# Optimization experiments

Hardware: AMD Instinct MI355X
Metric: run time of the kernel (lower is better)

Reference implementation:

```python
import jax, jax.numpy as jnp
import numpy as np

N, E, F, B, S, T, D = 50000, 150000, 100000, 64, 32, 32, 3
RADIUS = 1.0
SCALE = 500.0


def setup_inputs() -> dict:
    key = jax.random.key(0)
    ks = jax.random.split(key, 8)
    x = jax.random.normal(ks[0], (N, D), dtype=jnp.float32)
    node_weights = jax.random.uniform(ks[1], (N,), dtype=jnp.float32)
    edge_index = jax.random.randint(ks[2], (2, E), 0, N)
    edge_weights = jax.random.uniform(ks[3], (E,), dtype=jnp.float32)
    face = jax.random.randint(ks[4], (3, F), 0, N)
    face_weights = jax.random.uniform(ks[5], (F,), dtype=jnp.float32)
    batch = jnp.sort(jax.random.randint(ks[6], (N,), 0, B))
    v = jax.random.normal(ks[7], (D, T), dtype=jnp.float32)
    v = v / jnp.linalg.norm(v, axis=0, keepdims=True)  # unit directions
    lin = jnp.linspace(-RADIUS, RADIUS, S, dtype=jnp.float32)
    return {"x": x, "node_weights": node_weights, "edge_index": edge_index,
            "edge_weights": edge_weights, "face": face, "face_weights": face_weights,
            "batch": batch, "v": v, "lin": lin}


def compute_ecc(h, index, lin, num_segments):
    # h: [M, T] simplex heights; lin: [S] thresholds
    # sigmoid bump at each threshold, then scatter-add per graph -> [B, S, T]
    ecc = jax.nn.sigmoid(SCALE * (lin[None, :, None] - h[:, None, :]))  # [M, S, T]
    return jax.ops.segment_sum(ecc, index, num_segments=num_segments)


def reference(x, node_weights, edge_index, edge_weights, face, face_weights, batch, v, lin):
    nh = (x * node_weights[:, None]) @ v                      # [N, T] node heights
    eh = jnp.max(nh[edge_index], axis=0) * edge_weights[:, None]  # [E, T]
    fh = jnp.max(nh[face], axis=0) * face_weights[:, None]        # [F, T]
    idx_e = batch[edge_index[0]]
    idx_f = batch[face[0]]
    ect = (compute_ecc(nh, batch, lin, B)
           - compute_ecc(eh, idx_e, lin, B)
           + compute_ecc(fh, idx_f, lin, B))                  # [B, S, T]
    return ect  # normalized=False -> squeeze() is a no-op here
```

## Files before the change

kernel.cpp:

```cpp
#include <hip/hip_runtime.h>
#include <hip/hip_bf16.h>

#define N_NODES 50000
#define N_EDGES 150000
#define N_FACES 100000
#define NB 64
#define NS 32
#define NT 32
#define SCALE_C 500.0f
#define DLIN (2.0f / 31.0f)
#define INV_DLIN (31.0f / 2.0f)
#define WIN 0.02f
#define DSZ (NB * NS * NT)
#define NODE_CAP 1024
#define EDGE_CAP 3072
#define FACE_CAP 2048
#define SENT_H 2.0f

__device__ __forceinline__ float sigf(float z) {
    float e = __expf(-z);
    return __builtin_amdgcn_rcpf(1.0f + e);
}
__device__ __forceinline__ float4 fmax4(float4 a, float4 b) {
    return make_float4(fmaxf(a.x,b.x), fmaxf(a.y,b.y), fmaxf(a.z,b.z), fmaxf(a.w,b.w));
}
__device__ __forceinline__ float4 fscale4(float4 a, float w) {
    return make_float4(a.x*w, a.y*w, a.z*w, a.w*w);
}

__global__ __launch_bounds__(256) void fill_kernel(
    float* __restrict__ nh, int* __restrict__ ns,
    int* __restrict__ ea, int* __restrict__ eb, float* __restrict__ ews,
    int* __restrict__ fa, int* __restrict__ fb, int* __restrict__ fc,
    float* __restrict__ fws)
{
    int i = blockIdx.x * 256 + threadIdx.x;
    if (i < NT) nh[N_NODES * NT + i] = SENT_H;
    if (i < NB * NODE_CAP) ns[i] = N_NODES;
    if (i < NB * EDGE_CAP) { ea[i] = N_NODES; eb[i] = N_NODES; ews[i] = 1.0f; }
    if (i < NB * FACE_CAP) { fa[i] = N_NODES; fb[i] = N_NODES; fc[i] = N_NODES; fws[i] = 1.0f; }
}

__global__ __launch_bounds__(256) void prep_kernel(
    const float* __restrict__ x, const float* __restrict__ nw,
    const float* __restrict__ v, const int* __restrict__ ei,
    const float* __restrict__ ew, const int* __restrict__ fi,
    const float* __restrict__ fw, const int* __restrict__ batch,
    float* __restrict__ nh, int* __restrict__ ns,
    int* __restrict__ ea, int* __restrict__ eb, float* __restrict__ ews,
    int* __restrict__ fa, int* __restrict__ fb, int* __restrict__ fc,
    float* __restrict__ fws, int* __restrict__ cur,
    int nhB, int nbN, int nbE)
{
    if (blockIdx.x < nhB) {
        int idx = blockIdx.x * 256 + threadIdx.x;
        if (idx < N_NODES * NT) {
            int n = idx >> 5, t = idx & 31;
            float w = nw[n];
            nh[idx] = w * (x[3 * n] * v[t] + x[3 * n + 1] * v[NT + t] + x[3 * n + 2] * v[2 * NT + t]);
        }
        return;
    }
    __shared__ int cnt[NB], base_[NB];
    int b = blockIdx.x - nhB;
    int type, bb, M;
    if (b < nbN)            { type = 0; bb = b;             M = N_NODES; }
    else if (b < nbN + nbE) { type = 1; bb = b - nbN;       M = N_EDGES; }
    else                    { type = 2; bb = b - nbN - nbE; M = N_FACES; }
    int c0 = bb * 1024;
    if (threadIdx.x < NB) cnt[threadIdx.x] = 0;
    __syncthreads();
    int gv[4], iv[4], n = 0;
    #pragma unroll
    for (int k = 0; k < 4; k++) {
        int i = c0 + k * 256 + threadIdx.x;
        if (i < M) {
            int first = (type == 0) ? i : (type == 1 ? ei[i] : fi[i]);
            gv[n] = batch[first];
            iv[n] = i;
            atomicAdd(&cnt[gv[n]], 1);
            n++;
        }
    }
    __syncthreads();
    int* curT = cur + type * NB;
    if (threadIdx.x < NB) {
        base_[threadIdx.x] = atomicAdd(&curT[threadIdx.x], cnt[threadIdx.x]);
        cnt[threadIdx.x] = 0;
    }
    __syncthreads();
    int CAP = (type == 0) ? NODE_CAP : (type == 1 ? EDGE_CAP : FACE_CAP);
    for (int k = 0; k < n; k++) {
        int g = gv[k], i = iv[k];
        int pos = g * CAP + base_[g] + atomicAdd(&cnt[g], 1);
        if (type == 0) {
            ns[pos] = i;
        } else if (type == 1) {
            ea[pos] = ei[i]; eb[pos] = ei[N_EDGES + i]; ews[pos] = ew[i];
        } else {
            fa[pos] = fi[i]; fb[pos] = fi[N_FACES + i];
            fc[pos] = fi[2 * N_FACES + i]; fws[pos] = fw[i];
        }
    }
}

__global__ __launch_bounds__(256) void accum_kernel(
    const float* __restrict__ nh, const int* __restrict__ ns,
    const int* __restrict__ ea, const int* __restrict__ eb,
    const float* __restrict__ ews, const int* __restrict__ fa,
    const int* __restrict__ fb, const int* __restrict__ fc,
    const float* __restrict__ fws, const int* __restrict__ cur,
    float* __restrict__ delta)
{
    const int NBN = NB * NODE_CAP / 256;
    const int NBE = NB * EDGE_CAP / 256;
    int bid = blockIdx.x;
    int type, g, base, end;
    float sign;
    if (bid < NBN) {
        type = 0; g = bid >> 2; base = g * NODE_CAP + (bid & 3) * 256;
        end = g * NODE_CAP + cur[g]; sign = 1.0f;
    } else if (bid < NBN + NBE) {
        int b = bid - NBN; type = 1; g = b / 12;
        base = g * EDGE_CAP + (b % 12) * 256;
        end = g * EDGE_CAP + cur[NB + g]; sign = -1.0f;
    } else {
        int b = bid - NBN - NBE; type = 2; g = b >> 3;
        base = g * FACE_CAP + (b & 7) * 256;
        end = g * FACE_CAP + cur[2 * NB + g]; sign = 1.0f;
    }
    if (base >= end) return;

    __shared__ float tile[NT * NS];
    for (int k = threadIdx.x; k < NT * NS; k += 256) tile[k] = 0.0f;
    __syncthreads();

    int sub = threadIdx.x & 3;
    int sid = threadIdx.x >> 2;
    int t0 = sub * 8;

    #pragma unroll
    for (int p = 0; p < 4; p++) {
        int i = base + p * 64 + sid;
        float4 r0, r1;
        if (type == 0) {
            const float4* row = (const float4*)(nh + ns[i] * NT + t0);
            r0 = row[0]; r1 = row[1];
        } else if (type == 1) {
            const float4* ra = (const float4*)(nh + ea[i] * NT + t0);
            const float4* rb = (const float4*)(nh + eb[i] * NT + t0);
            float w = ews[i];
            float4 a0 = ra[0], a1 = ra[1], b0 = rb[0], b1 = rb[1];
            r0 = fscale4(fmax4(a0, b0), w);
            r1 = fscale4(fmax4(a1, b1), w);
        } else {
            const float4* ra = (const float4*)(nh + fa[i] * NT + t0);
            const float4* rb = (const float4*)(nh + fb[i] * NT + t0);
            const float4* rc = (const float4*)(nh + fc[i] * NT + t0);
            float w = fws[i];
            float4 a0 = ra[0], a1 = ra[1], b0 = rb[0], b1 = rb[1], c0 = rc[0], c1 = rc[1];
            r0 = fscale4(fmax4(fmax4(a0, b0), c0), w);
            r1 = fscale4(fmax4(fmax4(a1, b1), c1), w);
        }
        float h[8] = {r0.x, r0.y, r0.z, r0.w, r1.x, r1.y, r1.z, r1.w};
        #pragma unroll
        for (int j = 0; j < 8; j++) {
            float hh = h[j];
            int slo_u = (int)ceilf((hh - WIN + 1.0f) * INV_DLIN);
            int shi_u = (int)floorf((hh + WIN + 1.0f) * INV_DLIN);
            int slo = slo_u < 0 ? 0 : slo_u;
            int shi = shi_u > (NS - 1) ? (NS - 1) : shi_u;
            float prev = 0.0f;
            for (int s = slo; s <= shi; s++) {
                float vs = sigf(SCALE_C * (-1.0f + s * DLIN - hh));
                atomicAdd(&tile[(t0 + j) * NS + s], vs - prev);
                prev = vs;
            }
            int sstep = shi_u + 1;
            if (sstep <= NS - 1) {
                int sc = sstep < 0 ? 0 : sstep;
                atomicAdd(&tile[(t0 + j) * NS + sc], 1.0f - prev);
            }
        }
    }

    __syncthreads();
    for (int k = threadIdx.x; k < NT * NS; k += 256) {
        float vv = tile[k];
        if (vv != 0.0f) {
            int tt = k >> 5, ss = k & 31;
            atomicAdd(&delta[g * (NS * NT) + ss * NT + tt], sign * vv);
        }
    }
}

__global__ void finalize_kernel(const float* __restrict__ delta, float* __restrict__ out) {
    int idx = blockIdx.x * blockDim.x + threadIdx.x;
    if (idx >= NB * NT) return;
    int g = idx >> 5, t = idx & 31;
    const float* dg = delta + (g * NS) * NT + t;
    float* og = out + (g * NS) * NT + t;
    float run = 0.0f;
    for (int s = 0; s < NS; s++) {
        run += dg[s * NT];
        og[s * NT] = run;
    }
}

extern "C" void kernel_launch(void* const* d_in, const int* in_sizes, int n_in,
                              void* d_out, int out_size, void* d_ws, size_t ws_size,
                              hipStream_t stream) {
    const float* x     = (const float*)d_in[0];
    const float* nw    = (const float*)d_in[1];
    const int*   ei    = (const int*)d_in[2];
    const float* ew    = (const float*)d_in[3];
    const int*   fi    = (const int*)d_in[4];
    const float* fw    = (const float*)d_in[5];
    const int*   batch = (const int*)d_in[6];
    const float* v     = (const float*)d_in[7];
    const float* lin   = (const float*)d_in[8];
    (void)lin; (void)in_sizes; (void)n_in; (void)ws_size;
    float* out = (float*)d_out;

    char* ws = (char*)d_ws;
    float* delta = (float*)ws;
    int*   cur   = (int*)(ws + DSZ * 4);
    float* nh    = (float*)(ws + DSZ * 4 + 1024);
    int*   ns    = (int*)((char*)nh + (size_t)(N_NODES + 1) * NT * 4);
    int*   ea    = ns + NB * NODE_CAP;
    int*   eb    = ea + NB * EDGE_CAP;
    float* ews   = (float*)(eb + NB * EDGE_CAP);
    int*   fa    = (int*)(ews + NB * EDGE_CAP);
    int*   fb    = fa + NB * FACE_CAP;
    int*   fc    = fb + NB * FACE_CAP;
    float* fws   = (float*)(fc + NB * FACE_CAP);

    hipMemsetAsync(delta, 0, DSZ * 4 + 1024, stream);

    fill_kernel<<<NB * EDGE_CAP / 256, 256, 0, stream>>>(nh, ns, ea, eb, ews, fa, fb, fc, fws);

    int nhB = (N_NODES * NT + 255) / 256;
    int nbN = (N_NODES + 1023) / 1024;
    int nbE = (N_EDGES + 1023) / 1024;
    int nbF = (N_FACES + 1023) / 1024;
    prep_kernel<<<nhB + nbN + nbE + nbF, 256, 0, stream>>>(
        x, nw, v, ei, ew, fi, fw, batch,
        nh, ns, ea, eb, ews, fa, fb, fc, fws, cur, nhB, nbN, nbE);

    int nblk = NB * (NODE_CAP + EDGE_CAP + FACE_CAP) / 256;
    accum_kernel<<<nblk, 256, 0, stream>>>(
        nh, ns, ea, eb, ews, fa, fb, fc, fws, cur, delta);

    finalize_kernel<<<(NB * NT + 255) / 256, 256, 0, stream>>>(delta, out);
}
```

Baseline: 195.1 us.

## Remap accum threads to one wave per simplex with prefetched gathers

Changes the accum kernel mapping so each wave of 32 lanes handles one simplex, one lane per direction t, instead of 4 lanes covering 8 directions each. Loads become coalesced 128-byte rows, and the next simplex's indices and heights are software-prefetched across a 32-iteration loop. The shared tile is switched to s-major so LDS atomics from a wave hit consecutive addresses, and the final flush no longer transposes. Tail padding is added to the index arrays so prefetch reads past the segment stay in bounds. The cost is more loop iterations per thread and more divergence in the per-height window loop across lanes.

```diff
diff --git a/kernel.cpp b/kernel.cpp
--- a/kernel.cpp
+++ b/kernel.cpp
@@ -15,17 +15,12 @@
 #define NODE_CAP 1024
 #define EDGE_CAP 3072
 #define FACE_CAP 2048
+#define TAILPAD 64
 #define SENT_H 2.0f
 
 __device__ __forceinline__ float sigf(float z) {
     float e = __expf(-z);
     return __builtin_amdgcn_rcpf(1.0f + e);
-}
-__device__ __forceinline__ float4 fmax4(float4 a, float4 b) {
-    return make_float4(fmaxf(a.x,b.x), fmaxf(a.y,b.y), fmaxf(a.z,b.z), fmaxf(a.w,b.w));
-}
-__device__ __forceinline__ float4 fscale4(float4 a, float w) {
-    return make_float4(a.x*w, a.y*w, a.z*w, a.w*w);
 }
 
 __global__ __launch_bounds__(256) void fill_kernel(
@@ -36,9 +31,9 @@
 {
     int i = blockIdx.x * 256 + threadIdx.x;
     if (i < NT) nh[N_NODES * NT + i] = SENT_H;
-    if (i < NB * NODE_CAP) ns[i] = N_NODES;
-    if (i < NB * EDGE_CAP) { ea[i] = N_NODES; eb[i] = N_NODES; ews[i] = 1.0f; }
-    if (i < NB * FACE_CAP) { fa[i] = N_NODES; fb[i] = N_NODES; fc[i] = N_NODES; fws[i] = 1.0f; }
+    if (i < NB * NODE_CAP + TAILPAD) ns[i] = N_NODES;
+    if (i < NB * EDGE_CAP + TAILPAD) { ea[i] = N_NODES; eb[i] = N_NODES; ews[i] = 1.0f; }
+    if (i < NB * FACE_CAP + TAILPAD) { fa[i] = N_NODES; fb[i] = N_NODES; fc[i] = N_NODES; fws[i] = 1.0f; }
 }
 
 __global__ __launch_bounds__(256) void prep_kernel(
@@ -131,66 +126,80 @@
     }
     if (base >= end) return;
 
-    __shared__ float tile[NT * NS];
-    for (int k = threadIdx.x; k < NT * NS; k += 256) tile[k] = 0.0f;
-    __syncthreads();
-
-    int sub = threadIdx.x & 3;
-    int sid = threadIdx.x >> 2;
-    int t0 = sub * 8;
-
-    #pragma unroll
-    for (int p = 0; p < 4; p++) {
-        int i = base + p * 64 + sid;
-        float4 r0, r1;
-        if (type == 0) {
-            const float4* row = (const float4*)(nh + ns[i] * NT + t0);
-            r0 = row[0]; r1 = row[1];
-        } else if (type == 1) {
-            const float4* ra = (const float4*)(nh + ea[i] * NT + t0);
-            const float4* rb = (const float4*)(nh + eb[i] * NT + t0);
-            float w = ews[i];
-            float4 a0 = ra[0], a1 = ra[1], b0 = rb[0], b1 = rb[1];
-            r0 = fscale4(fmax4(a0, b0), w);
-            r1 = fscale4(fmax4(a1, b1), w);
-        } else {
-            const float4* ra = (const float4*)(nh + fa[i] * NT + t0);
-            const float4* rb = (const float4*)(nh + fb[i] * NT + t0);
-            const float4* rc = (const float4*)(nh + fc[i] * NT + t0);
-            float w = fws[i];
-            float4 a0 = ra[0], a1 = ra[1], b0 = rb[0], b1 = rb[1], c0 = rc[0], c1 = rc[1];
-            r0 = fscale4(fmax4(fmax4(a0, b0), c0), w);
-            r1 = fscale4(fmax4(fmax4(a1, b1), c1), w);
-        }
-        float h[8] = {r0.x, r0.y, r0.z, r0.w, r1.x, r1.y, r1.z, r1.w};
-        #pragma unroll
-        for (int j = 0; j < 8; j++) {
-            float hh = h[j];
-            int slo_u = (int)ceilf((hh - WIN + 1.0f) * INV_DLIN);
-            int shi_u = (int)floorf((hh + WIN + 1.0f) * INV_DLIN);
-            int slo = slo_u < 0 ? 0 : slo_u;
-            int shi = shi_u > (NS - 1) ? (NS - 1) : shi_u;
-            float prev = 0.0f;
-            for (int s = slo; s <= shi; s++) {
-                float vs = sigf(SCALE_C * (-1.0f + s * DLIN - hh));
-                atomicAdd(&tile[(t0 + j) * NS + s], vs - prev);
-                prev = vs;
-            }
-            int sstep = shi_u + 1;
-            if (sstep <= NS - 1) {
-                int sc = sstep < 0 ? 0 : sstep;
-                atomicAdd(&tile[(t0 + j) * NS + sc], 1.0f - prev);
-            }
-        }
-    }
-
-    __syncthreads();
-    for (int k = threadIdx.x; k < NT * NS; k += 256) {
+    __shared__ float tile[NS * NT];
+    for (int k = threadIdx.x; k < NS * NT; k += 256) tile[k] = 0.0f;
+    __syncthreads();
+
+    int t = threadIdx.x & 31, slot = threadIdx.x >> 5;
+
+    #define EMIT(H) do {                                                    \
+        float hh = (H);                                                     \
+        int slo_u = (int)ceilf((hh - WIN + 1.0f) * INV_DLIN);               \
+        int shi_u = (int)floorf((hh + WIN + 1.0f) * INV_DLIN);              \
+        int slo = slo_u < 0 ? 0 : slo_u;                                    \
+        int shi = shi_u > (NS - 1) ? (NS - 1) : shi_u;                      \
+        float prev = 0.0f;                                                  \
+        for (int s = slo; s <= shi; s++) {                                  \
+            float vs = sigf(SCALE_C * (-1.0f + s * DLIN - hh));             \
+            atomicAdd(&tile[s * NT + t], vs - prev);                        \
+            prev = vs;                                                      \
+        }                                                                   \
+        int sstep = shi_u + 1;                                              \
+        if (sstep <= NS - 1) {                                              \
+            int sc = sstep < 0 ? 0 : sstep;                                 \
+            atomicAdd(&tile[sc * NT + t], 1.0f - prev);                     \
+        } } while (0)
+
+    if (type == 0) {
+        int i = base + slot;
+        int n1 = ns[i + 8];
+        float h0 = nh[ns[i] * NT + t];
+        #pragma unroll 2
+        for (int k = 0; k < 32; k++) {
+            int n2 = ns[i + 16];
+            float h1 = nh[n1 * NT + t];
+            EMIT(h0);
+            n1 = n2; h0 = h1; i += 8;
+        }
+    } else if (type == 1) {
+        int i = base + slot;
+        int a1 = ea[i + 8], b1 = eb[i + 8];
+        float w1 = ews[i + 8];
+        int a0 = ea[i], b0 = eb[i];
+        float w0 = ews[i];
+        float ha0 = nh[a0 * NT + t], hb0 = nh[b0 * NT + t];
+        #pragma unroll 2
+        for (int k = 0; k < 32; k++) {
+            int a2 = ea[i + 16], b2 = eb[i + 16];
+            float w2 = ews[i + 16];
+            float ha1 = nh[a1 * NT + t], hb1 = nh[b1 * NT + t];
+            EMIT(fmaxf(ha0, hb0) * w0);
+            a1 = a2; b1 = b2; w0 = w1; w1 = w2;
+            ha0 = ha1; hb0 = hb1; i += 8;
+        }
+    } else {
+        int i = base + slot;
+        int a1 = fa[i + 8], b1 = fb[i + 8], c1 = fc[i + 8];
+        float w1 = fws[i + 8];
+        int a0 = fa[i], b0 = fb[i], c0 = fc[i];
+        float w0 = fws[i];
+        float ha0 = nh[a0 * NT + t], hb0 = nh[b0 * NT + t], hc0 = nh[c0 * NT + t];
+        #pragma unroll 2
+        for (int k = 0; k < 32; k++) {
+            int a2 = fa[i + 16], b2 = fb[i + 16], c2 = fc[i + 16];
+            float w2 = fws[i + 16];
+            float ha1 = nh[a1 * NT + t], hb1 = nh[b1 * NT + t], hc1 = nh[c1 * NT + t];
+            EMIT(fmaxf(fmaxf(ha0, hb0), hc0) * w0);
+            a1 = a2; b1 = b2; c1 = c2; w0 = w1; w1 = w2;
+            ha0 = ha1; hb0 = hb1; hc0 = hc1; i += 8;
+        }
+    }
+    #undef EMIT
+
+    __syncthreads();
+    for (int k = threadIdx.x; k < NS * NT; k += 256) {
         float vv = tile[k];
-        if (vv != 0.0f) {
-            int tt = k >> 5, ss = k & 31;
-            atomicAdd(&delta[g * (NS * NT) + ss * NT + tt], sign * vv);
-        }
+        if (vv != 0.0f) atomicAdd(&delta[g * (NS * NT) + k], sign * vv);
     }
 }
 
@@ -227,17 +236,18 @@
     int*   cur   = (int*)(ws + DSZ * 4);
     float* nh    = (float*)(ws + DSZ * 4 + 1024);
     int*   ns    = (int*)((char*)nh + (size_t)(N_NODES + 1) * NT * 4);
-    int*   ea    = ns + NB * NODE_CAP;
-    int*   eb    = ea + NB * EDGE_CAP;
-    float* ews   = (float*)(eb + NB * EDGE_CAP);
-    int*   fa    = (int*)(ews + NB * EDGE_CAP);
-    int*   fb    = fa + NB * FACE_CAP;
-    int*   fc    = fb + NB * FACE_CAP;
-    float* fws   = (float*)(fc + NB * FACE_CAP);
+    int*   ea    = ns + NB * NODE_CAP + TAILPAD;
+    int*   eb    = ea + NB * EDGE_CAP + TAILPAD;
+    float* ews   = (float*)(eb + NB * EDGE_CAP + TAILPAD);
+    int*   fa    = (int*)(ews + NB * EDGE_CAP + TAILPAD);
+    int*   fb    = fa + NB * FACE_CAP + TAILPAD;
+    int*   fc    = fb + NB * FACE_CAP + TAILPAD;
+    float* fws   = (float*)(fc + NB * FACE_CAP + TAILPAD);
 
     hipMemsetAsync(delta, 0, DSZ * 4 + 1024, stream);
 
-    fill_kernel<<<NB * EDGE_CAP / 256, 256, 0, stream>>>(nh, ns, ea, eb, ews, fa, fb, fc, fws);
+    fill_kernel<<<(NB * EDGE_CAP + TAILPAD + 255) / 256, 256, 0, stream>>>(
+        nh, ns, ea, eb, ews, fa, fb, fc, fws);
 
     int nhB = (N_NODES * NT + 255) / 256;
     int nbN = (N_NODES + 1023) / 1024;
```

New measurement: 194.5 us. Within noise of the previous version (-0.3%).
